# Performance work log

Hardware: AMD Instinct MI355X
Metric: run time of the kernel (lower is better)

## Reference

```python
import jax, jax.numpy as jnp
import numpy as np

EPS = 1e-5

def layernorm(x, g, b):
    mu = jnp.mean(x, axis=-1, keepdims=True)
    var = jnp.mean(jnp.square(x - mu), axis=-1, keepdims=True)
    return (x - mu) * jax.lax.rsqrt(var + EPS) * g + b

def setup_inputs() -> dict:
    key = jax.random.key(0)
    B, T, C, H = 4, 2048, 1024, 16
    hs = C // H
    ks = jax.random.split(key, 16)
    s_in = 0.02
    return {
        "x": jax.random.normal(ks[0], (B, T, C), jnp.float32),
        "ln1_g": jnp.ones((C,), jnp.float32),
        "ln1_b": jnp.zeros((C,), jnp.float32),
        "Wq": jax.random.normal(ks[1], (H, C, hs), jnp.float32) * s_in,
        "Wk": jax.random.normal(ks[2], (H, C, hs), jnp.float32) * s_in,
        "Wv": jax.random.normal(ks[3], (H, C, hs), jnp.float32) * s_in,
        "Wo": jax.random.normal(ks[4], (C, C), jnp.float32) * s_in,
        "bo": jnp.zeros((C,), jnp.float32),
        "ln2_g": jnp.ones((C,), jnp.float32),
        "ln2_b": jnp.zeros((C,), jnp.float32),
        "W1": jax.random.normal(ks[5], (C, 4 * C), jnp.float32) * s_in,
        "b1": jnp.zeros((4 * C,), jnp.float32),
        "W2": jax.random.normal(ks[6], (4 * C, C), jnp.float32) * s_in,
        "b2": jnp.zeros((C,), jnp.float32),
    }

def reference(x, ln1_g, ln1_b, Wq, Wk, Wv, Wo, bo, ln2_g, ln2_b, W1, b1, W2, b2):
    B, T, C = x.shape
    H, _, hs = Wq.shape
    # --- multi-head causal self-attention on LN1(x) ---
    h = layernorm(x, ln1_g, ln1_b)
    q = jnp.einsum('btc,hcs->bhts', h, Wq)
    k = jnp.einsum('btc,hcs->bhts', h, Wk)
    v = jnp.einsum('btc,hcs->bhts', h, Wv)
    scores = jnp.einsum('bhqs,bhks->bhqk', q, k) * (hs ** -0.5)
    causal = jnp.tril(jnp.ones((T, T), bool))
    scores = jnp.where(causal, scores, -jnp.inf)
    attn = jax.nn.softmax(scores, axis=-1)  # dropout p=0 -> identity
    out = jnp.einsum('bhqk,bhks->bhqs', attn, v)
    out = out.transpose(0, 2, 1, 3).reshape(B, T, H * hs)  # concat heads
    x = x + out @ Wo + bo
    # --- feed-forward on LN2(x) ---
    h2 = layernorm(x, ln2_g, ln2_b)
    ff = jax.nn.relu(h2 @ W1 + b1) @ W2 + b2
    return x + ff
```

## Files before the change

kernel.cpp:

```cpp
#include <hip/hip_runtime.h>
#include <math.h>

#define B_  4
#define T_  2048
#define C_  1024
#define H_  16
#define HS_ 64
#define BT_ (B_*T_)
#define F_  (4*C_)
#define N3_ (3*C_)

typedef unsigned short ushort_t;
typedef __attribute__((ext_vector_type(4))) unsigned short us4;
typedef __attribute__((ext_vector_type(8))) unsigned short us8;
typedef __attribute__((ext_vector_type(4))) float f32x4;
typedef __attribute__((ext_vector_type(8))) __bf16 bf16x8;

__device__ __forceinline__ float bf2f(ushort_t u) {
    union { unsigned int i; float f; } c; c.i = ((unsigned int)u) << 16; return c.f;
}
__device__ __forceinline__ ushort_t f2bf(float f) {
    union { unsigned int i; float f; } c; c.f = f;
    unsigned int i = c.i;
    return (ushort_t)((i + 0x7FFFu + ((i >> 16) & 1u)) >> 16);
}

#define GLB_(p) ((const __attribute__((address_space(1))) unsigned int*)(size_t)(p))
#define LDS_(p) ((__attribute__((address_space(3))) unsigned int*)(unsigned int)(size_t)(p))
__device__ __forceinline__ void gload16(const void* g, void* l) {
    __builtin_amdgcn_global_load_lds(GLB_(g), LDS_(l), 16, 0, 0);
}

template<int N> __device__ __forceinline__ void vm_wait() {
    if constexpr (N >= 8)      asm volatile("s_waitcnt vmcnt(8)" ::: "memory");
    else if constexpr (N == 6) asm volatile("s_waitcnt vmcnt(6)" ::: "memory");
    else if constexpr (N == 4) asm volatile("s_waitcnt vmcnt(4)" ::: "memory");
    else if constexpr (N == 3) asm volatile("s_waitcnt vmcnt(3)" ::: "memory");
    else                       asm volatile("s_waitcnt vmcnt(0)" ::: "memory");
}

__global__ __launch_bounds__(256) void repack_qkv_k(
    const float* __restrict__ Wq, const float* __restrict__ Wk,
    const float* __restrict__ Wv, ushort_t* __restrict__ WtB)
{
    __shared__ float tile[64][65];
    int bid = blockIdx.x;
    int p  = bid >> 8;
    int h  = (bid >> 4) & 15;
    int c0 = (bid & 15) * 64;
    const float* W = (p == 0) ? Wq : ((p == 1) ? Wk : Wv);
    int t = threadIdx.x;
    int cl = t >> 2, seg = (t & 3) * 16;
    const float* src = W + ((size_t)h * C_ + c0 + cl) * HS_ + seg;
#pragma unroll
    for (int i = 0; i < 4; i++) {
        float4 v = *(const float4*)(src + i * 4);
        tile[cl][seg + i*4 + 0] = v.x; tile[cl][seg + i*4 + 1] = v.y;
        tile[cl][seg + i*4 + 2] = v.z; tile[cl][seg + i*4 + 3] = v.w;
    }
    __syncthreads();
    int sl = t >> 2;
    int n = p * C_ + h * HS_ + sl;
    ushort_t* dst = WtB + (size_t)n * C_ + c0 + seg;
    us8 o0, o1;
#pragma unroll
    for (int e = 0; e < 8; e++) { o0[e] = f2bf(tile[seg + e][sl]); o1[e] = f2bf(tile[seg + 8 + e][sl]); }
    *(us8*)dst = o0; *(us8*)(dst + 8) = o1;
}

__global__ __launch_bounds__(256) void transpose_k(
    const float* __restrict__ in, ushort_t* __restrict__ out, int K, int N)
{
    __shared__ float tile[64][65];
    int n0 = blockIdx.x * 64, k0 = blockIdx.y * 64;
    int t = threadIdx.x;
    int kl = t >> 2, seg = (t & 3) * 16;
    const float* src = in + (size_t)(k0 + kl) * N + n0 + seg;
#pragma unroll
    for (int i = 0; i < 4; i++) {
        float4 v = *(const float4*)(src + i * 4);
        tile[kl][seg + i*4 + 0] = v.x; tile[kl][seg + i*4 + 1] = v.y;
        tile[kl][seg + i*4 + 2] = v.z; tile[kl][seg + i*4 + 3] = v.w;
    }
    __syncthreads();
    int nl = t >> 2;
    ushort_t* dst = out + (size_t)(n0 + nl) * K + k0 + seg;
    us8 o0, o1;
#pragma unroll
    for (int e = 0; e < 8; e++) { o0[e] = f2bf(tile[seg + e][nl]); o1[e] = f2bf(tile[seg + 8 + e][nl]); }
    *(us8*)dst = o0; *(us8*)(dst + 8) = o1;
}

__global__ __launch_bounds__(256) void transv_k(
    const ushort_t* __restrict__ QKV, ushort_t* __restrict__ Vt)
{
    __shared__ ushort_t tl[64][72];
    int bid = blockIdx.x;
    int tt = bid & 31;
    int bh = bid >> 5;
    int b  = bh >> 4;
    int h  = bh & 15;
    int t = threadIdx.x;
    int r = t >> 2, sg = (t & 3) * 16;
    const ushort_t* src = QKV + (size_t)(b * T_ + tt * 64 + r) * N3_ + 2 * C_ + h * HS_ + sg;
    us8 a0 = *(const us8*)src;
    us8 a1 = *(const us8*)(src + 8);
#pragma unroll
    for (int e = 0; e < 8; e++) { tl[r][sg + e] = a0[e]; tl[r][sg + 8 + e] = a1[e]; }
    __syncthreads();
    ushort_t* dst = Vt + ((size_t)(b * H_ + h) * HS_ + r) * T_ + tt * 64 + sg;
    us8 o0, o1;
#pragma unroll
    for (int e = 0; e < 8; e++) { o0[e] = tl[sg + e][r]; o1[e] = tl[sg + 8 + e][r]; }
    *(us8*)dst = o0; *(us8*)(dst + 8) = o1;
}

template<int IN_BF16>
__global__ __launch_bounds__(256) void ln_k(
    const void* __restrict__ xv, const float* __restrict__ g,
    const float* __restrict__ b, ushort_t* __restrict__ out)
{
    int row = blockIdx.x;
    int t = threadIdx.x;
    float v[4];
    if (IN_BF16) {
        const ushort_t* xr = (const ushort_t*)xv + (size_t)row * C_;
        us4 u = *(const us4*)(xr + t * 4);
#pragma unroll
        for (int i = 0; i < 4; i++) v[i] = bf2f(u[i]);
    } else {
        const float* xr = (const float*)xv + (size_t)row * C_;
        float4 f = *(const float4*)(xr + t * 4);
        v[0] = f.x; v[1] = f.y; v[2] = f.z; v[3] = f.w;
    }
    float s  = v[0] + v[1] + v[2] + v[3];
    float ss = v[0]*v[0] + v[1]*v[1] + v[2]*v[2] + v[3]*v[3];
#pragma unroll
    for (int off = 32; off > 0; off >>= 1) {
        s  += __shfl_xor(s, off);
        ss += __shfl_xor(ss, off);
    }
    __shared__ float red[8];
    int wv = t >> 6;
    if ((t & 63) == 0) { red[wv*2] = s; red[wv*2+1] = ss; }
    __syncthreads();
    s  = red[0] + red[2] + red[4] + red[6];
    ss = red[1] + red[3] + red[5] + red[7];
    float mu  = s * (1.0f / C_);
    float var = ss * (1.0f / C_) - mu * mu;
    float rs  = rsqrtf(var + 1e-5f);
    float4 gv = *(const float4*)(g + t * 4);
    float4 bv = *(const float4*)(b + t * 4);
    us4 o;
    o[0] = f2bf((v[0] - mu) * rs * gv.x + bv.x);
    o[1] = f2bf((v[1] - mu) * rs * gv.y + bv.y);
    o[2] = f2bf((v[2] - mu) * rs * gv.z + bv.z);
    o[3] = f2bf((v[3] - mu) * rs * gv.w + bv.w);
    *(us4*)(out + (size_t)row * C_ + t * 4) = o;
}

template<int MI, int RELU, int BIAS, int RES_MODE, int OUT_BF16>
__global__ __launch_bounds__(512) void mgemm8_k(
    const ushort_t* __restrict__ A, const ushort_t* __restrict__ Bw,
    const float* __restrict__ bias, const void* __restrict__ res,
    void* __restrict__ out, int M, int N, int K, int lda)
{
    constexpr int BM = MI * 32;
    constexpr int A_LOADS = (MI == 8) ? 2 : 1;
    constexpr int UNIT = A_LOADS + 2;
    __shared__ ushort_t As[MI * 4096];
    __shared__ ushort_t Bs[32768];

    int tid = threadIdx.x;
    int l = tid & 63, w = tid >> 6;
    int wm = w >> 2, wn = w & 3;
    int m0 = blockIdx.y * BM, n0 = blockIdx.x * 256;
    const int nt = K >> 6;

    auto stageA = [&](int tile, int kh) {
        ushort_t* dst = As + ((tile & 1) * 2 + kh) * (BM * 32);
#pragma unroll
        for (int inst = 0; inst < A_LOADS; ++inst) {
            int slot = inst * 512 + tid;
            int row = slot >> 2, q = slot & 3;
            const ushort_t* src = A + (size_t)(m0 + row) * lda + tile * 64 + kh * 32
                                  + ((q ^ (row & 3)) * 8);
            gload16(src, dst + (inst * 512 + w * 64) * 8);
        }
    };
    auto stageB = [&](int tile, int kh) {
        ushort_t* dst = Bs + ((tile & 1) * 2 + kh) * 8192;
#pragma unroll
        for (int inst = 0; inst < 2; ++inst) {
            int slot = inst * 512 + tid;
            int row = slot >> 2, q = slot & 3;
            const ushort_t* src = Bw + (size_t)(n0 + row) * K + tile * 64 + kh * 32
                                  + ((q ^ (row & 3)) * 8);
            gload16(src, dst + (inst * 512 + w * 64) * 8);
        }
    };

    f32x4 acc[MI][4];
#pragma unroll
    for (int i = 0; i < MI; i++)
#pragma unroll
        for (int j = 0; j < 4; j++) acc[i][j] = (f32x4){0.f, 0.f, 0.f, 0.f};

    stageA(0, 0); stageB(0, 0);
    stageA(0, 1); stageB(0, 1);
    stageA(1, 0); stageB(1, 0);

    for (int t = 0; t < nt; ++t) {
        int buf = t & 1;
#pragma unroll
        for (int kh = 0; kh < 2; ++kh) {
            if (t == nt - 1) { if (kh == 0) vm_wait<UNIT>(); else vm_wait<0>(); }
            else vm_wait<2 * UNIT>();
            __builtin_amdgcn_s_barrier();
            __builtin_amdgcn_sched_barrier(0);

            const ushort_t* Ab = As + (buf * 2 + kh) * (BM * 32);
            const ushort_t* Bb = Bs + (buf * 2 + kh) * 8192;
            bf16x8 af[MI], bf[4];
#pragma unroll
            for (int i = 0; i < MI; ++i) {
                int row = wm * (BM / 2) + i * 16 + (l & 15);
                af[i] = *(const bf16x8*)(Ab + row * 32 + (((l >> 4) ^ (row & 3)) * 8));
            }
#pragma unroll
            for (int j = 0; j < 4; ++j) {
                int row = wn * 64 + j * 16 + (l & 15);
                bf[j] = *(const bf16x8*)(Bb + row * 32 + (((l >> 4) ^ (row & 3)) * 8));
            }
            if (kh == 0) { if (t + 1 < nt) { stageA(t + 1, 1); stageB(t + 1, 1); } }
            else         { if (t + 2 < nt) { stageA(t + 2, 0); stageB(t + 2, 0); } }

            __builtin_amdgcn_s_setprio(1);
#pragma unroll
            for (int i = 0; i < MI; ++i)
#pragma unroll
                for (int j = 0; j < 4; ++j)
                    acc[i][j] = __builtin_amdgcn_mfma_f32_16x16x32_bf16(af[i], bf[j], acc[i][j], 0, 0, 0);
            __builtin_amdgcn_s_setprio(0);
            __builtin_amdgcn_sched_barrier(0);
            __builtin_amdgcn_s_barrier();
        }
    }

    int colb = n0 + wn * 64 + (l & 15);
    int rowb = m0 + wm * (BM / 2) + ((l >> 4) << 2);
#pragma unroll
    for (int j = 0; j < 4; j++) {
        int col = colb + j * 16;
        float bval = BIAS ? bias[col] : 0.f;
#pragma unroll
        for (int i = 0; i < MI; i++) {
#pragma unroll
            for (int r = 0; r < 4; r++) {
                int row = rowb + i * 16 + r;
                float v = acc[i][j][r] + bval;
                if (RELU) v = fmaxf(v, 0.f);
                size_t idx = (size_t)row * N + col;
                if (RES_MODE == 1) v += ((const float*)res)[idx];
                else if (RES_MODE == 2) v += bf2f(((const ushort_t*)res)[idx]);
                if (OUT_BF16) ((ushort_t*)out)[idx] = f2bf(v);
                else          ((float*)out)[idx]    = v;
            }
        }
    }
}

__global__ __launch_bounds__(256) void fattn_k(
    ushort_t* __restrict__ QKV, const ushort_t* __restrict__ Vt)
{
    __shared__ ushort_t Qs[64 * 64];
    __shared__ ushort_t Ks[2][64 * 64];
    __shared__ ushort_t Vs[2][64 * 64];
    __shared__ ushort_t Ps[64 * 64];
    int bid = blockIdx.x;
    int pr = bid & 15;
    int bh = bid >> 4;
    int b  = bh >> 4;
    int h  = bh & 15;
    int tid = threadIdx.x;
    int lid = tid & 63, w = tid >> 6;

    int srow = w * 16 + (lid >> 3);
    int sseg0 = (lid & 7) ^ (srow & 7);
    int sseg1 = (lid & 7) ^ ((srow + 8) & 7);
    const ushort_t* Kg = QKV + (size_t)(b * T_) * N3_ + C_ + h * HS_;
    const ushort_t* Vg = Vt + (size_t)(b * H_ + h) * HS_ * T_;

    int mrow = w * 16 + (lid & 15);
    int fseg = lid >> 4;
    int qlocb = w * 16 + ((lid >> 4) << 2);

    const __bf16 oneb = (__bf16)1.0f;
    bf16x8 ones = {oneb, oneb, oneb, oneb, oneb, oneb, oneb, oneb};

    for (int half = 0; half < 2; ++half) {
        int qt = half ? (31 - pr) : pr;
        const ushort_t* Qg = QKV + (size_t)(b * T_ + qt * 64) * N3_ + h * HS_;

        __syncthreads();
        gload16(Qg + (size_t)srow * N3_ + sseg0 * 8,       Qs + w * 1024);
        gload16(Qg + (size_t)(srow + 8) * N3_ + sseg1 * 8, Qs + w * 1024 + 512);
        gload16(Kg + (size_t)srow * N3_ + sseg0 * 8,       Ks[0] + w * 1024);
        gload16(Kg + (size_t)(srow + 8) * N3_ + sseg1 * 8, Ks[0] + w * 1024 + 512);
        gload16(Vg + (size_t)srow * T_ + sseg0 * 8,        Vs[0] + w * 1024);
        gload16(Vg + (size_t)(srow + 8) * T_ + sseg1 * 8,  Vs[0] + w * 1024 + 512);

        f32x4 accO[4];
#pragma unroll
        for (int j = 0; j < 4; j++) accO[j] = (f32x4){0.f, 0.f, 0.f, 0.f};
        f32x4 accL = (f32x4){0.f, 0.f, 0.f, 0.f};

        for (int kt = 0; kt <= qt; ++kt) {
            int cur = kt & 1;
            __syncthreads();
            if (kt < qt) {
                int nk = kt + 1;
                gload16(Kg + (size_t)(nk * 64 + srow) * N3_ + sseg0 * 8,     Ks[cur ^ 1] + w * 1024);
                gload16(Kg + (size_t)(nk * 64 + srow + 8) * N3_ + sseg1 * 8, Ks[cur ^ 1] + w * 1024 + 512);
                gload16(Vg + (size_t)srow * T_ + nk * 64 + sseg0 * 8,        Vs[cur ^ 1] + w * 1024);
                gload16(Vg + (size_t)(srow + 8) * T_ + nk * 64 + sseg1 * 8,  Vs[cur ^ 1] + w * 1024 + 512);
            }
            const ushort_t* Kc = Ks[cur];
            const ushort_t* Vc = Vs[cur];

            f32x4 s[4];
#pragma unroll
            for (int j = 0; j < 4; j++) s[j] = (f32x4){0.f, 0.f, 0.f, 0.f};
            __builtin_amdgcn_s_setprio(1);
#pragma unroll
            for (int ks = 0; ks < 2; ks++) {
                bf16x8 aq = *(const bf16x8*)(Qs + mrow * 64 + (((ks * 4 + fseg) ^ (mrow & 7)) * 8));
#pragma unroll
                for (int j = 0; j < 4; j++) {
                    int krow = j * 16 + (lid & 15);
                    bf16x8 bk = *(const bf16x8*)(Kc + krow * 64 + (((ks * 4 + fseg) ^ (krow & 7)) * 8));
                    s[j] = __builtin_amdgcn_mfma_f32_16x16x32_bf16(aq, bk, s[j], 0, 0, 0);
                }
            }
            __builtin_amdgcn_s_setprio(0);

            bool diag = (kt == qt);
#pragma unroll
            for (int r = 0; r < 4; r++) {
                int qabs = qt * 64 + qlocb + r;
                int qloc = qlocb + r;
#pragma unroll
                for (int j = 0; j < 4; j++) {
                    int kabs = kt * 64 + j * 16 + (lid & 15);
                    float p = (diag && kabs > qabs) ? 0.f : __expf(s[j][r] * 0.125f);
                    int col = j * 16 + (lid & 15);
                    Ps[qloc * 64 + (((col >> 3) ^ (qloc & 7)) * 8) + (col & 7)] = f2bf(p);
                }
            }

            __builtin_amdgcn_s_setprio(1);
#pragma unroll
            for (int ks = 0; ks < 2; ks++) {
                bf16x8 ap = *(const bf16x8*)(Ps + mrow * 64 + (((ks * 4 + fseg) ^ (mrow & 7)) * 8));
                accL = __builtin_amdgcn_mfma_f32_16x16x32_bf16(ap, ones, accL, 0, 0, 0);
#pragma unroll
                for (int j = 0; j < 4; j++) {
                    int drow = j * 16 + (lid & 15);
                    bf16x8 bv = *(const bf16x8*)(Vc + drow * 64 + (((ks * 4 + fseg) ^ (drow & 7)) * 8));
                    accO[j] = __builtin_amdgcn_mfma_f32_16x16x32_bf16(ap, bv, accO[j], 0, 0, 0);
                }
            }
            __builtin_amdgcn_s_setprio(0);
        }

#pragma unroll
        for (int r = 0; r < 4; r++) {
            float inv = 1.0f / accL[r];
            int qabs = qt * 64 + qlocb + r;
            ushort_t* orow = QKV + (size_t)(b * T_ + qabs) * N3_ + h * HS_;
#pragma unroll
            for (int j = 0; j < 4; j++)
                orow[j * 16 + (lid & 15)] = f2bf(accO[j][r] * inv);
        }
    }
}

extern "C" void kernel_launch(void* const* d_in, const int* in_sizes, int n_in,
                              void* d_out, int out_size, void* d_ws, size_t ws_size,
                              hipStream_t stream)
{
    const float* x   = (const float*)d_in[0];
    const float* g1  = (const float*)d_in[1];
    const float* be1 = (const float*)d_in[2];
    const float* Wq  = (const float*)d_in[3];
    const float* Wk  = (const float*)d_in[4];
    const float* Wv  = (const float*)d_in[5];
    const float* Wo  = (const float*)d_in[6];
    const float* bo  = (const float*)d_in[7];
    const float* g2  = (const float*)d_in[8];
    const float* be2 = (const float*)d_in[9];
    const float* W1  = (const float*)d_in[10];
    const float* b1  = (const float*)d_in[11];
    const float* W2  = (const float*)d_in[12];
    const float* b2  = (const float*)d_in[13];

    const size_t UB2 = (size_t)BT_ * C_ * 2;
    const size_t WT_B = (size_t)N3_ * C_ * 2;
    const size_t WO_B = (size_t)C_ * C_ * 2;
    const size_t W1_B = (size_t)C_ * F_ * 2;
    const size_t REQ = 5 * UB2 + WT_B + WO_B + 2 * W1_B;
    if (ws_size < REQ) {
        hipMemsetAsync(d_out, 0, (size_t)out_size * 4, stream);
        return;
    }
    char* wsb = (char*)d_ws;
    ushort_t* hB   = (ushort_t*)(wsb);
    ushort_t* qkvB = (ushort_t*)(wsb + UB2);
    ushort_t* ff1B = qkvB;
    ushort_t* WtB  = (ushort_t*)(wsb + 5 * UB2);
    ushort_t* WoB  = (ushort_t*)(wsb + 5 * UB2 + WT_B);
    ushort_t* W1B  = (ushort_t*)(wsb + 5 * UB2 + WT_B + WO_B);
    ushort_t* W2B  = (ushort_t*)(wsb + 5 * UB2 + WT_B + WO_B + W1_B);
    float* x2F = (float*)d_out;

    repack_qkv_k<<<3 * 16 * 16, 256, 0, stream>>>(Wq, Wk, Wv, WtB);
    transpose_k<<<dim3(C_ / 64, C_ / 64), 256, 0, stream>>>(Wo, WoB, C_, C_);
    transpose_k<<<dim3(F_ / 64, C_ / 64), 256, 0, stream>>>(W1, W1B, C_, F_);
    transpose_k<<<dim3(C_ / 64, F_ / 64), 256, 0, stream>>>(W2, W2B, F_, C_);

    ln_k<0><<<BT_, 256, 0, stream>>>(x, g1, be1, hB);
    mgemm8_k<8,0,0,0,1><<<dim3(N3_ / 256, BT_ / 256), 512, 0, stream>>>(
        hB, WtB, nullptr, nullptr, qkvB, BT_, N3_, C_, C_);
    transv_k<<<B_ * H_ * (T_ / 64), 256, 0, stream>>>(qkvB, hB);
    fattn_k<<<B_ * H_ * 16, 256, 0, stream>>>(qkvB, hB);
    mgemm8_k<4,0,1,1,0><<<dim3(C_ / 256, BT_ / 128), 512, 0, stream>>>(
        qkvB, WoB, bo, x, x2F, BT_, C_, C_, N3_);
    ln_k<0><<<BT_, 256, 0, stream>>>(x2F, g2, be2, hB);
    mgemm8_k<8,1,1,0,1><<<dim3(F_ / 256, BT_ / 256), 512, 0, stream>>>(
        hB, W1B, b1, nullptr, ff1B, BT_, F_, C_, C_);
    mgemm8_k<4,0,1,1,0><<<dim3(C_ / 256, BT_ / 128), 512, 0, stream>>>(
        ff1B, W2B, b2, x2F, (float*)d_out, BT_, C_, F_, F_);
}
```

Before: 406.7 us.

## Generalize GEMM tiling template and use 128x128 tiles for N=1024 GEMMs

The GEMM kernel is now templated on block tile sizes and warp layout instead of a fixed 256-wide N tile. The two N=1024 GEMMs (Wo projection and W2) switch from 128x256 tiles with 512 threads to 128x128 tiles with 256 threads, which doubles their block count to improve CU occupancy and wave balance. The LDS swizzle also changes from row&3 to (row>>1)&3 to alter bank-conflict behaviour. Smaller tiles reduce operand reuse per block, and the fixed vm_wait counts now depend on each config issuing exactly two loads per stage.

```diff
diff --git a/kernel.cpp b/kernel.cpp
--- a/kernel.cpp
+++ b/kernel.cpp
@@ -159,52 +159,54 @@
     *(us4*)(out + (size_t)row * C_ + t * 4) = o;
 }
 
-template<int MI, int RELU, int BIAS, int RES_MODE, int OUT_BF16>
-__global__ __launch_bounds__(512) void mgemm8_k(
+template<int BM, int BN, int WM, int WN, int RELU, int BIAS, int RES_MODE, int OUT_BF16>
+__global__ __launch_bounds__(WM * WN * 64) void mgemm8_k(
     const ushort_t* __restrict__ A, const ushort_t* __restrict__ Bw,
     const float* __restrict__ bias, const void* __restrict__ res,
     void* __restrict__ out, int M, int N, int K, int lda)
 {
-    constexpr int BM = MI * 32;
-    constexpr int A_LOADS = (MI == 8) ? 2 : 1;
-    constexpr int UNIT = A_LOADS + 2;
-    __shared__ ushort_t As[MI * 4096];
-    __shared__ ushort_t Bs[32768];
+    constexpr int THREADS = WM * WN * 64;
+    constexpr int MIa = BM / WM / 16;
+    constexpr int MIb = BN / WN / 16;
+    constexpr int A_INSTS = (BM * 64) / (16 * THREADS);
+    constexpr int B_INSTS = (BN * 64) / (16 * THREADS);
+    __shared__ ushort_t As[4 * BM * 32];
+    __shared__ ushort_t Bs[4 * BN * 32];
 
     int tid = threadIdx.x;
     int l = tid & 63, w = tid >> 6;
-    int wm = w >> 2, wn = w & 3;
-    int m0 = blockIdx.y * BM, n0 = blockIdx.x * 256;
+    int wm = w / WN, wn = w % WN;
+    int m0 = blockIdx.y * BM, n0 = blockIdx.x * BN;
     const int nt = K >> 6;
 
     auto stageA = [&](int tile, int kh) {
         ushort_t* dst = As + ((tile & 1) * 2 + kh) * (BM * 32);
 #pragma unroll
-        for (int inst = 0; inst < A_LOADS; ++inst) {
-            int slot = inst * 512 + tid;
+        for (int inst = 0; inst < A_INSTS; ++inst) {
+            int slot = inst * THREADS + tid;
             int row = slot >> 2, q = slot & 3;
             const ushort_t* src = A + (size_t)(m0 + row) * lda + tile * 64 + kh * 32
-                                  + ((q ^ (row & 3)) * 8);
-            gload16(src, dst + (inst * 512 + w * 64) * 8);
+                                  + ((q ^ ((row >> 1) & 3)) * 8);
+            gload16(src, dst + (inst * THREADS + w * 64) * 8);
         }
     };
     auto stageB = [&](int tile, int kh) {
-        ushort_t* dst = Bs + ((tile & 1) * 2 + kh) * 8192;
-#pragma unroll
-        for (int inst = 0; inst < 2; ++inst) {
-            int slot = inst * 512 + tid;
+        ushort_t* dst = Bs + ((tile & 1) * 2 + kh) * (BN * 32);
+#pragma unroll
+        for (int inst = 0; inst < B_INSTS; ++inst) {
+            int slot = inst * THREADS + tid;
             int row = slot >> 2, q = slot & 3;
             const ushort_t* src = Bw + (size_t)(n0 + row) * K + tile * 64 + kh * 32
-                                  + ((q ^ (row & 3)) * 8);
-            gload16(src, dst + (inst * 512 + w * 64) * 8);
+                                  + ((q ^ ((row >> 1) & 3)) * 8);
+            gload16(src, dst + (inst * THREADS + w * 64) * 8);
         }
     };
 
-    f32x4 acc[MI][4];
-#pragma unroll
-    for (int i = 0; i < MI; i++)
-#pragma unroll
-        for (int j = 0; j < 4; j++) acc[i][j] = (f32x4){0.f, 0.f, 0.f, 0.f};
+    f32x4 acc[MIa][MIb];
+#pragma unroll
+    for (int i = 0; i < MIa; i++)
+#pragma unroll
+        for (int j = 0; j < MIb; j++) acc[i][j] = (f32x4){0.f, 0.f, 0.f, 0.f};
 
     stageA(0, 0); stageB(0, 0);
     stageA(0, 1); stageB(0, 1);
@@ -214,32 +216,32 @@
         int buf = t & 1;
 #pragma unroll
         for (int kh = 0; kh < 2; ++kh) {
-            if (t == nt - 1) { if (kh == 0) vm_wait<UNIT>(); else vm_wait<0>(); }
-            else vm_wait<2 * UNIT>();
+            if (t == nt - 1) { if (kh == 0) vm_wait<4>(); else vm_wait<0>(); }
+            else vm_wait<8>();
             __builtin_amdgcn_s_barrier();
             __builtin_amdgcn_sched_barrier(0);
 
             const ushort_t* Ab = As + (buf * 2 + kh) * (BM * 32);
-            const ushort_t* Bb = Bs + (buf * 2 + kh) * 8192;
-            bf16x8 af[MI], bf[4];
-#pragma unroll
-            for (int i = 0; i < MI; ++i) {
-                int row = wm * (BM / 2) + i * 16 + (l & 15);
-                af[i] = *(const bf16x8*)(Ab + row * 32 + (((l >> 4) ^ (row & 3)) * 8));
-            }
-#pragma unroll
-            for (int j = 0; j < 4; ++j) {
-                int row = wn * 64 + j * 16 + (l & 15);
-                bf[j] = *(const bf16x8*)(Bb + row * 32 + (((l >> 4) ^ (row & 3)) * 8));
+            const ushort_t* Bb = Bs + (buf * 2 + kh) * (BN * 32);
+            bf16x8 af[MIa], bf[MIb];
+#pragma unroll
+            for (int i = 0; i < MIa; ++i) {
+                int row = wm * (BM / WM) + i * 16 + (l & 15);
+                af[i] = *(const bf16x8*)(Ab + row * 32 + (((l >> 4) ^ ((row >> 1) & 3)) * 8));
+            }
+#pragma unroll
+            for (int j = 0; j < MIb; ++j) {
+                int row = wn * (BN / WN) + j * 16 + (l & 15);
+                bf[j] = *(const bf16x8*)(Bb + row * 32 + (((l >> 4) ^ ((row >> 1) & 3)) * 8));
             }
             if (kh == 0) { if (t + 1 < nt) { stageA(t + 1, 1); stageB(t + 1, 1); } }
             else         { if (t + 2 < nt) { stageA(t + 2, 0); stageB(t + 2, 0); } }
 
             __builtin_amdgcn_s_setprio(1);
 #pragma unroll
-            for (int i = 0; i < MI; ++i)
-#pragma unroll
-                for (int j = 0; j < 4; ++j)
+            for (int i = 0; i < MIa; ++i)
+#pragma unroll
+                for (int j = 0; j < MIb; ++j)
                     acc[i][j] = __builtin_amdgcn_mfma_f32_16x16x32_bf16(af[i], bf[j], acc[i][j], 0, 0, 0);
             __builtin_amdgcn_s_setprio(0);
             __builtin_amdgcn_sched_barrier(0);
@@ -247,14 +249,14 @@
         }
     }
 
-    int colb = n0 + wn * 64 + (l & 15);
-    int rowb = m0 + wm * (BM / 2) + ((l >> 4) << 2);
-#pragma unroll
-    for (int j = 0; j < 4; j++) {
+    int colb = n0 + wn * (BN / WN) + (l & 15);
+    int rowb = m0 + wm * (BM / WM) + ((l >> 4) << 2);
+#pragma unroll
+    for (int j = 0; j < MIb; j++) {
         int col = colb + j * 16;
         float bval = BIAS ? bias[col] : 0.f;
 #pragma unroll
-        for (int i = 0; i < MI; i++) {
+        for (int i = 0; i < MIa; i++) {
 #pragma unroll
             for (int r = 0; r < 4; r++) {
                 int row = rowb + i * 16 + r;
@@ -429,15 +431,15 @@
     transpose_k<<<dim3(C_ / 64, F_ / 64), 256, 0, stream>>>(W2, W2B, F_, C_);
 
     ln_k<0><<<BT_, 256, 0, stream>>>(x, g1, be1, hB);
-    mgemm8_k<8,0,0,0,1><<<dim3(N3_ / 256, BT_ / 256), 512, 0, stream>>>(
+    mgemm8_k<256,256,2,4,0,0,0,1><<<dim3(N3_ / 256, BT_ / 256), 512, 0, stream>>>(
         hB, WtB, nullptr, nullptr, qkvB, BT_, N3_, C_, C_);
     transv_k<<<B_ * H_ * (T_ / 64), 256, 0, stream>>>(qkvB, hB);
     fattn_k<<<B_ * H_ * 16, 256, 0, stream>>>(qkvB, hB);
-    mgemm8_k<4,0,1,1,0><<<dim3(C_ / 256, BT_ / 128), 512, 0, stream>>>(
+    mgemm8_k<128,128,2,2,0,1,1,0><<<dim3(C_ / 128, BT_ / 128), 256, 0, stream>>>(
         qkvB, WoB, bo, x, x2F, BT_, C_, C_, N3_);
     ln_k<0><<<BT_, 256, 0, stream>>>(x2F, g2, be2, hB);
-    mgemm8_k<8,1,1,0,1><<<dim3(F_ / 256, BT_ / 256), 512, 0, stream>>>(
+    mgemm8_k<256,256,2,4,1,1,0,1><<<dim3(F_ / 256, BT_ / 256), 512, 0, stream>>>(
         hB, W1B, b1, nullptr, ff1B, BT_, F_, C_, C_);
-    mgemm8_k<4,0,1,1,0><<<dim3(C_ / 256, BT_ / 128), 512, 0, stream>>>(
+    mgemm8_k<128,128,2,2,0,1,1,0><<<dim3(C_ / 128, BT_ / 128), 256, 0, stream>>>(
         ff1B, W2B, b2, x2F, (float*)d_out, BT_, C_, F_, F_);
 }
```

Result: no change. 400.2 us (-1.6%).
